# Performance work log

Hardware: AMD Instinct MI355X
Metric: run time of the kernel (lower is better)

The kernel has to match this reference:

```python
import jax, jax.numpy as jnp
import numpy as np

EPS = 1e-5
SLOPE = 0.01  # nn.LeakyReLU default
K = 32
SIGMA = 1.0

def lrelu(x):
    return jnp.where(x >= 0, x, SLOPE * x)

def bn(x, gamma, beta, axes):
    # BatchNorm in training mode (fresh module, batch statistics)
    mu = jnp.mean(x, axis=axes, keepdims=True)
    var = jnp.var(x, axis=axes, keepdims=True)
    return (x - mu) * jax.lax.rsqrt(var + EPS) * gamma + beta

def knn_gather(x, k):
    # x: (B, N, C) -> neighbor features (B, N, k, C) by smallest squared distance
    sq = jnp.sum(x * x, axis=-1)
    d = sq[:, :, None] - 2.0 * jnp.einsum('bnc,bmc->bnm', x, x) + sq[:, None, :]
    idx = jax.lax.top_k(-d, k)[1]                      # (B, N, k)
    nbr = jax.vmap(lambda xb, ib: xb[ib])(x, idx)      # (B, N, k, C)
    return nbr

def edge_conv(x, w1, g1, b1, w2, g2, b2):
    # DGCNN EdgeConv: feat = [x_j - x_i, x_i] -> 1x1 conv/BN/LeakyReLU x2 -> max over k
    nbr = knn_gather(x, K)                             # (B, N, k, C)
    xc = x[:, :, None, :]
    feat = jnp.concatenate([nbr - xc, jnp.broadcast_to(xc, nbr.shape)], axis=-1)
    h = lrelu(bn(jnp.einsum('bnkc,oc->bnko', feat, w1), g1, b1, (0, 1, 2)))
    h = lrelu(bn(jnp.einsum('bnkc,oc->bnko', h, w2), g2, b2, (0, 1, 2)))
    return jnp.max(h, axis=2)                          # (B, N, C_out)

def gaussian_kernel_conv(xnei, centers):
    # xnei: (B, N, k, C), centers: (O, C) -> (B, N, O)
    d = (jnp.sum(xnei * xnei, -1)[..., None]
         - 2.0 * jnp.einsum('bnkc,oc->bnko', xnei, centers)
         + jnp.sum(centers * centers, -1))
    return jnp.sum(jnp.exp(-d / (2.0 * SIGMA ** 2)), axis=2)

def setup_inputs() -> dict:
    key = jax.random.key(0)
    ks = jax.random.split(key, 16)
    s = 0.05
    return {
        'x': jax.random.normal(ks[0], (2, 3, 64, 64), jnp.float32),
        'kc_centers': jax.random.normal(ks[1], (128, 3), jnp.float32),
        'e1_w1': jax.random.normal(ks[2], (64, 6), jnp.float32) * s,
        'e1_g1': jnp.ones((64,), jnp.float32), 'e1_b1': jnp.zeros((64,), jnp.float32),
        'e1_w2': jax.random.normal(ks[3], (64, 64), jnp.float32) * s,
        'e1_g2': jnp.ones((64,), jnp.float32), 'e1_b2': jnp.zeros((64,), jnp.float32),
        'e2_w1': jax.random.normal(ks[4], (128, 128), jnp.float32) * s,
        'e2_g1': jnp.ones((128,), jnp.float32), 'e2_b1': jnp.zeros((128,), jnp.float32),
        'e2_w2': jax.random.normal(ks[5], (128, 128), jnp.float32) * s,
        'e2_g2': jnp.ones((128,), jnp.float32), 'e2_b2': jnp.zeros((128,), jnp.float32),
        'w1': jax.random.normal(ks[6], (1024, 256), jnp.float32) * s,
        'g1': jnp.ones((1024,), jnp.float32), 'b1': jnp.zeros((1024,), jnp.float32),
        'w2': jax.random.normal(ks[7], (512, 1024), jnp.float32) * s,
        'g2': jnp.ones((512,), jnp.float32), 'b2': jnp.zeros((512,), jnp.float32),
        'w3': jax.random.normal(ks[8], (256, 512), jnp.float32) * s,
        'g3': jnp.ones((256,), jnp.float32), 'b3': jnp.zeros((256,), jnp.float32),
        'w4': jax.random.normal(ks[9], (9, 256), jnp.float32) * s,
    }

def reference(x, kc_centers, e1_w1, e1_g1, e1_b1, e1_w2, e1_g2, e1_b2,
              e2_w1, e2_g1, e2_b1, e2_w2, e2_g2, e2_b2,
              w1, g1, b1, w2, g2, b2, w3, g3, b3, w4):
    bs, f, c, n = x.shape
    # knn over the (B, c*n, 3) point cloud
    pts = x.reshape(bs, -1, c * n).transpose(0, 2, 1)
    xnei = knn_gather(pts, K)                               # (B, c*n, K, 3)
    kernels = gaussian_kernel_conv(xnei, kc_centers)        # (B, c*n, 128)
    # EdgeConv chain on reshape-view (matches torch reshape semantics exactly)
    xe = x.reshape(bs, c * n, -1)                           # (B, c*n, 3)
    xe = edge_conv(xe, e1_w1, e1_g1, e1_b1, e1_w2, e1_g2, e1_b2)   # (B, c*n, 64)
    xe = edge_conv(xe, e2_w1, e2_g1, e2_b1, e2_w2, e2_g2, e2_b2)   # (B, c*n, 128)
    h = jnp.concatenate([xe.reshape(bs, -1, c, n),
                         kernels.transpose(0, 2, 1).reshape(bs, -1, c, n)], axis=1)  # (B,256,c,n)
    def cbr(h, w, g, b):
        h = jnp.einsum('bchw,oc->bohw', h, w)               # 1x1 conv, no bias
        return lrelu(bn(h, g[None, :, None, None], b[None, :, None, None], (0, 2, 3)))
    h = cbr(h, w1, g1, b1)
    h = cbr(h, w2, g2, b2)
    h = cbr(h, w3, g3, b3)
    h = jnp.einsum('bchw,oc->bohw', h, w4)                  # (B, 9, c, n)
    h = jnp.max(jnp.max(h, axis=3), axis=2)                 # (B, 9)
    out = h + jnp.eye(3, dtype=h.dtype).reshape(1, 9)
    return out.reshape(bs, 3, 3)
```

## Files before the change

kernel.cpp:

```cpp
#include <hip/hip_runtime.h>
#include <hip/hip_fp16.h>
#include <math.h>

#define WN 4096
#define NP 8192
#define KK 32
#define EPSB 1e-5f

typedef __attribute__((ext_vector_type(8))) short s8v;
typedef __attribute__((ext_vector_type(4))) float f4v;

__device__ __forceinline__ float lrelu(float x){ return fmaxf(x, 0.01f*x); }
__device__ __forceinline__ float rlane(float v, int c){
  return __int_as_float(__builtin_amdgcn_readlane(__float_as_int(v), c));
}
__device__ __forceinline__ short f2bf(float f){
  unsigned u = __float_as_uint(f);
  u = (u + 0x7fffu + ((u>>16)&1u)) >> 16;
  return (short)u;
}

__global__ void k_prep(const float* __restrict__ x, float* __restrict__ pts, float* __restrict__ xe0,
                       float* __restrict__ sqp, float* __restrict__ sqe,
                       float4* __restrict__ pts4, float4* __restrict__ xe04){
  int i = blockIdx.x*256 + threadIdx.x;
  if(i >= NP) return;
  int b = i>>12, p = i&4095;
  const float* xb = x + b*12288;
  float a0 = xb[p], a1 = xb[4096+p], a2 = xb[8192+p];
  pts[i*3+0]=a0; pts[i*3+1]=a1; pts[i*3+2]=a2;
  float sp = (a0*a0 + a1*a1) + a2*a2;
  sqp[i] = sp;
  pts4[i] = make_float4(a0,a1,a2,sp);
  float e0 = xb[p*3+0], e1 = xb[p*3+1], e2 = xb[p*3+2];
  xe0[i*3+0]=e0; xe0[i*3+1]=e1; xe0[i*3+2]=e2;
  float se = (e0*e0 + e1*e1) + e2*e2;
  sqe[i] = se;
  xe04[i] = make_float4(e0,e1,e2,se);
}

__device__ __forceinline__ void bitonic64(float& d, int& m, int l){
  #pragma unroll
  for(int k=2;k<=64;k<<=1){
    #pragma unroll
    for(int j=k>>1;j>0;j>>=1){
      float pd = __shfl_xor(d, j);
      int pm = __shfl_xor(m, j);
      bool pLess = (pd < d);
      bool dirUp = ((l & k) == 0);
      bool lower = ((l & j) == 0);
      bool take = dirUp ? (lower ? pLess : !pLess) : (lower ? !pLess : pLess);
      if(take){ d = pd; m = pm; }
    }
  }
}

__device__ __forceinline__ void topk_stream(float d, int m, int l, float& lv, int& li){
  unsigned long long mask = __ballot(d < rlane(lv, 31));
  while(mask){
    int s = __ffsll((unsigned long long)mask) - 1;
    float cd = __shfl(d, s);
    int cm = __shfl(m, s);
    unsigned long long less = __ballot(lv < cd);
    int pos = __popcll(less & 0xffffffffULL);
    float uv = __shfl_up(lv, 1);
    int ui = __shfl_up(li, 1);
    if(l < 32){
      if(l == pos){ lv = cd; li = cm; }
      else if(l > pos){ lv = uv; li = ui; }
    }
    mask &= mask - 1;
  }
}

__global__ __launch_bounds__(256) void k_knn3(const float4* __restrict__ pnt4, int* __restrict__ idx){
  int l = threadIdx.x&63;
  int q = blockIdx.x*4 + (threadIdx.x>>6);
  int b = q>>12, qr = q&4095;
  const float4* pb = pnt4 + ((size_t)b<<12);
  float4 qv = pb[qr];
  float q0=qv.x, q1=qv.y, q2=qv.z, sqq=qv.w;
  float4 nc = pb[l + 64];
  float dd; int mm = l;
  {
    float4 c = pb[l];
    float dot = q0*c.x + q1*c.y + q2*c.z;
    dd = (sqq - 2.0f*dot) + c.w;
  }
  bitonic64(dd, mm, l);
  float lv = (l<32) ? dd : 3.4e38f;
  int li = (l<32) ? mm : 0x7fffffff;
  #pragma unroll 4
  for(int j=1;j<64;j++){
    float4 c = nc;
    nc = pb[l + (((j+1)&63)<<6)];
    float dot = q0*c.x + q1*c.y + q2*c.z;
    float d = (sqq - 2.0f*dot) + c.w;
    topk_stream(d, l + (j<<6), l, lv, li);
  }
  if(l < 32) idx[(size_t)q*KK + l] = li;
}

__global__ __launch_bounds__(256) void k_knn_sel(const __half2* __restrict__ D, int* __restrict__ idx){
  int l = threadIdx.x&63;
  int q = blockIdx.x*4 + (threadIdx.x>>6);
  int b = q>>12, qr = q&4095;
  const __half2* row = D + ((size_t)b<<23) + ((size_t)qr<<11);
  __half2 h0 = row[l];
  __half2 nh = row[l + 64];
  float2 f0 = __half22float2(h0);
  float dmin, dmax; int mmin, mmax;
  if(f0.x <= f0.y){ dmin=f0.x; mmin=2*l;   dmax=f0.y; mmax=2*l+1; }
  else            { dmin=f0.y; mmin=2*l+1; dmax=f0.x; mmax=2*l;   }
  bitonic64(dmin, mmin, l);
  float lv = (l<32) ? dmin : 3.4e38f;
  int li = (l<32) ? mmin : 0x7fffffff;
  topk_stream(dmax, mmax, l, lv, li);
  #pragma unroll 4
  for(int j=1;j<32;j++){
    __half2 h = nh;
    nh = row[l + (((j+1)&31)<<6)];
    float2 g = __half22float2(h);
    int base = 2*(l + (j<<6));
    topk_stream(g.x, base,   l, lv, li);
    topk_stream(g.y, base+1, l, lv, li);
  }
  if(l < 32) idx[(size_t)q*KK + l] = li;
}

__global__ __launch_bounds__(128) void k_gauss(const float* __restrict__ pts, const float* __restrict__ sqp,
                                               const int* __restrict__ idxP, const float* __restrict__ cen,
                                               float* __restrict__ kout){
  __shared__ float nbx[KK], nby[KK], nbz[KK], nsq[KK];
  int p = blockIdx.x; int b = p>>12; int t = threadIdx.x;
  if(t < KK){
    int id = idxP[(size_t)p*KK + t] + (b<<12);
    nbx[t]=pts[id*3]; nby[t]=pts[id*3+1]; nbz[t]=pts[id*3+2];
    nsq[t]=sqp[id];
  }
  __syncthreads();
  float c0=cen[t*3], c1=cen[t*3+1], c2=cen[t*3+2];
  float sqc=(c0*c0+c1*c1)+c2*c2;
  float acc=0.f;
  #pragma unroll
  for(int k=0;k<KK;k++){
    float dot = nbx[k]*c0 + nby[k]*c1 + nbz[k]*c2;
    float d = (nsq[k] - 2.0f*dot) + sqc;
    acc += __expf(-0.5f*d);
  }
  kout[(size_t)((b<<7)+t)*4096 + (p&4095)] = acc;
}

__global__ void k_fin(const float* __restrict__ psum, const float* __restrict__ psq, int NW, int C, float Nn,
                      const float* __restrict__ g, const float* __restrict__ be,
                      float* __restrict__ sc, float* __restrict__ sh){
  int o = blockIdx.x, t = threadIdx.x;
  float s=0.f, q=0.f;
  for(int w=t; w<NW; w+=256){ s += psum[(size_t)w*C+o]; q += psq[(size_t)w*C+o]; }
  __shared__ float ls[256], lq[256];
  ls[t]=s; lq[t]=q; __syncthreads();
  for(int st=128; st; st>>=1){ if(t<st){ ls[t]+=ls[t+st]; lq[t]+=lq[t+st]; } __syncthreads(); }
  if(t==0){
    float mu = ls[0]/Nn;
    float var = lq[0]/Nn - mu*mu; if(var<0.f) var=0.f;
    float s1 = g[o]*rsqrtf(var + EPSB);
    sc[o]=s1; sh[o]=be[o]-mu*s1;
  }
}

__global__ __launch_bounds__(256) void k_ec1mom(const float* __restrict__ xe0, const int* __restrict__ idx1,
                                                float* __restrict__ pmom){
  int tid = blockIdx.x*256 + threadIdx.x;
  int l = threadIdx.x & 63;
  int wid = tid >> 6;
  float a[27];
  #pragma unroll
  for(int v=0;v<27;v++) a[v]=0.f;
  #pragma unroll
  for(int u=0;u<2;u++){
    int s = tid*2 + u;
    int p = s>>5;
    int bb = (p>>12)<<12;
    int id = bb + idx1[s];
    const float* nb = xe0 + (size_t)id*3;
    const float* xc = xe0 + (size_t)p*3;
    float f[6];
    f[0]=nb[0]-xc[0]; f[1]=nb[1]-xc[1]; f[2]=nb[2]-xc[2];
    f[3]=xc[0]; f[4]=xc[1]; f[5]=xc[2];
    int v=0;
    #pragma unroll
    for(int i=0;i<6;i++){
      #pragma unroll
      for(int j=i;j<6;j++){ a[v] = fmaf(f[i], f[j], a[v]); v++; }
    }
    #pragma unroll
    for(int i=0;i<6;i++) a[21+i] += f[i];
  }
  #pragma unroll
  for(int v=0;v<27;v++){
    float t = a[v];
    #pragma unroll
    for(int off=32; off; off>>=1) t += __shfl_xor(t, off);
    if(l==0) pmom[v*2048 + wid] = t;
  }
}

__global__ void k_msum(const float* __restrict__ pmom, float* __restrict__ mom){
  int v = blockIdx.x; int t = threadIdx.x;
  float s=0.f;
  for(int i=t;i<2048;i+=256) s += pmom[v*2048+i];
  __shared__ float ls[256];
  ls[t]=s; __syncthreads();
  for(int st=128; st; st>>=1){ if(t<st) ls[t]+=ls[t+st]; __syncthreads(); }
  if(t==0) mom[v]=ls[0];
}

__global__ void k_ec1bn(const float* __restrict__ mom, const float* __restrict__ w1,
                        const float* __restrict__ g, const float* __restrict__ be,
                        float* __restrict__ sc, float* __restrict__ sh){
  __shared__ float M[27];
  int t = threadIdx.x;
  if(t<27) M[t]=mom[t];
  __syncthreads();
  if(t<64){
    float w[6];
    #pragma unroll
    for(int c=0;c<6;c++) w[c]=w1[t*6+c];
    float qf=0.f, m1=0.f;
    int v=0;
    #pragma unroll
    for(int i=0;i<6;i++){
      #pragma unroll
      for(int j=i;j<6;j++){ qf += (i==j?1.f:2.f)*w[i]*w[j]*M[v]; v++; }
    }
    #pragma unroll
    for(int i=0;i<6;i++) m1 += w[i]*M[21+i];
    float N = 262144.f;
    float mu = m1/N;
    float var = qf/N - mu*mu; if(var<0.f) var=0.f;
    float s1 = g[t]*rsqrtf(var + EPSB);
    sc[t]=s1; sh[t]=be[t]-mu*s1;
  }
}

__global__ __launch_bounds__(256) void k_ec1g2(const float* __restrict__ xe0, const int* __restrict__ idx1,
                                               const float* __restrict__ w1, const float* __restrict__ w2T,
                                               const float* __restrict__ s1, const float* __restrict__ t1,
                                               float* __restrict__ h2m, float* __restrict__ psum,
                                               float* __restrict__ psq){
  __shared__ float As[64*64];
  __shared__ float Bs[64*132];
  __shared__ float feat[6][128];
  __shared__ float w1l[384];
  int t = threadIdx.x;
  int blk = blockIdx.x;
  int s0 = blk*128;
  int pbase = s0>>5;
  int bb = (s0>>17)<<12;
  #pragma unroll
  for(int i=0;i<16;i++) As[t + i*256] = w2T[t + i*256];
  for(int i=t; i<384; i+=256) w1l[i] = w1[i];
  if(t < 128){
    int s = s0 + t;
    int p = pbase + (t>>5);
    int id = bb + idx1[s];
    const float* nb = xe0 + (size_t)id*3;
    const float* xc = xe0 + (size_t)p*3;
    float x0 = xc[0], x1 = xc[1], x2 = xc[2];
    feat[0][t] = nb[0]-x0; feat[1][t] = nb[1]-x1; feat[2][t] = nb[2]-x2;
    feat[3][t] = x0; feat[4][t] = x1; feat[5][t] = x2;
  }
  __syncthreads();
  #pragma unroll
  for(int i=0;i<32;i++){
    int e = t + (i<<8);
    int k = e>>7, n = e&127;
    float h = w1l[k*6+0]*feat[0][n] + w1l[k*6+1]*feat[1][n] + w1l[k*6+2]*feat[2][n]
            + w1l[k*6+3]*feat[3][n] + w1l[k*6+4]*feat[4][n] + w1l[k*6+5]*feat[5][n];
    Bs[k*132 + n] = lrelu(fmaf(h, s1[k], t1[k]));
  }
  __syncthreads();
  int tx = t&15, ty = t>>4;
  float acc[4][8];
  #pragma unroll
  for(int i=0;i<4;i++){
    #pragma unroll
    for(int j=0;j<8;j++) acc[i][j]=0.f;
  }
  #pragma unroll 4
  for(int k=0;k<64;k++){
    float4 a  = *(const float4*)&As[k*64 + ty*4];
    float4 b0 = *(const float4*)&Bs[k*132 + tx*4];
    float4 b1 = *(const float4*)&Bs[k*132 + 64 + tx*4];
    float av[4] = {a.x,a.y,a.z,a.w};
    float bv[8] = {b0.x,b0.y,b0.z,b0.w,b1.x,b1.y,b1.z,b1.w};
    #pragma unroll
    for(int i=0;i<4;i++){
      #pragma unroll
      for(int j=0;j<8;j++) acc[i][j] = fmaf(av[i], bv[j], acc[i][j]);
    }
  }
  #pragma unroll
  for(int i=0;i<4;i++){
    int m = ty*4 + i;
    float sr = ((acc[i][0]+acc[i][1])+(acc[i][2]+acc[i][3])) + ((acc[i][4]+acc[i][5])+(acc[i][6]+acc[i][7]));
    float sq = ((acc[i][0]*acc[i][0]+acc[i][1]*acc[i][1])+(acc[i][2]*acc[i][2]+acc[i][3]*acc[i][3]))
             + ((acc[i][4]*acc[i][4]+acc[i][5]*acc[i][5])+(acc[i][6]*acc[i][6]+acc[i][7]*acc[i][7]));
    #pragma unroll
    for(int off=1; off<16; off<<=1){ sr += __shfl_xor(sr, off); sq += __shfl_xor(sq, off); }
    if(tx==0){ psum[(size_t)blk*64+m]=sr; psq[(size_t)blk*64+m]=sq; }
    float m0 = fmaxf(fmaxf(acc[i][0],acc[i][1]), fmaxf(acc[i][2],acc[i][3]));
    float m1 = fmaxf(fmaxf(acc[i][4],acc[i][5]), fmaxf(acc[i][6],acc[i][7]));
    #pragma unroll
    for(int off=1; off<8; off<<=1){ m0 = fmaxf(m0, __shfl_xor(m0, off)); m1 = fmaxf(m1, __shfl_xor(m1, off)); }
    if((tx&7)==0){
      int pl = pbase + (tx>>3);
      h2m[(size_t)pl*64 + m]     = m0;
      h2m[(size_t)(pl+2)*64 + m] = m1;
    }
  }
}

__global__ __launch_bounds__(256) void k_ec1fin(const float* __restrict__ h2m, const float* __restrict__ s2,
                                                const float* __restrict__ t2, float* __restrict__ xe1,
                                                float* __restrict__ xe1T, float* __restrict__ sqx){
  int gid = blockIdx.x*256 + threadIdx.x;
  int p = gid>>6, l = gid&63;
  float v = lrelu(fmaf(h2m[(size_t)p*64+l], s2[l], t2[l]));
  xe1[(size_t)p*64+l] = v;
  int b=p>>12, pr=p&4095;
  xe1T[(size_t)(b*64+l)*4096 + pr] = v;
  float sq = v*v;
  #pragma unroll
  for(int off=32; off; off>>=1) sq += __shfl_xor(sq, off);
  if(l==0) sqx[p]=sq;
}

__global__ __launch_bounds__(256) void k_dgemm_m(const short* __restrict__ X, const float* __restrict__ sqx,
                                                 __half* __restrict__ D){
  __shared__ short sA[8192], sB[8192];
  int t = threadIdx.x;
  int lane = t&63, w = t>>6;
  int wm4 = (w>>1)*4, wn4 = (w&1)*4;
  int mb = blockIdx.y, nb = blockIdx.x, b = blockIdx.z;
  const short* AG = X + (size_t)(b*32 + mb)*8192;
  const short* BG = X + (size_t)(b*32 + nb)*8192;
  #pragma unroll
  for(int i=0;i<4;i++){
    int slot = t + i*256;
    *(s8v*)&sA[slot*8] = *(const s8v*)&AG[slot*8];
    *(s8v*)&sB[slot*8] = *(const s8v*)&BG[slot*8];
  }
  __syncthreads();
  f4v acc[4][4];
  #pragma unroll
  for(int i=0;i<4;i++){
    #pragma unroll
    for(int j=0;j<4;j++) acc[i][j] = (f4v)(0.f);
  }
  #pragma unroll
  for(int kh=0;kh<2;kh++){
    s8v av[4], bv[4];
    #pragma unroll
    for(int f=0;f<4;f++) av[f] = *(const s8v*)&sA[(kh*8 + wm4 + f)*512 + lane*8];
    #pragma unroll
    for(int f=0;f<4;f++) bv[f] = *(const s8v*)&sB[(kh*8 + wn4 + f)*512 + lane*8];
    #pragma unroll
    for(int fm=0;fm<4;fm++){
      #pragma unroll
      for(int fn=0;fn<4;fn++)
        acc[fm][fn] = __builtin_amdgcn_mfma_f32_16x16x32_bf16(av[fm], bv[fn], acc[fm][fn], 0, 0, 0);
    }
  }
  const float* sb = sqx + (b<<12);
  __half* Db = D + ((size_t)b<<24);
  int l15 = lane&15, l4 = (lane>>4)*4;
  #pragma unroll
  for(int fm=0;fm<4;fm++){
    int m0 = mb*128 + wm4*16 + fm*16 + l4;
    float sm0 = sb[m0], sm1 = sb[m0+1], sm2 = sb[m0+2], sm3 = sb[m0+3];
    #pragma unroll
    for(int fn=0;fn<4;fn++){
      int n = nb*128 + wn4*16 + fn*16 + l15;
      float sqn = sb[n];
      __half2 h01 = __floats2half2_rn((sm0 + sqn) - 2.f*acc[fm][fn][0],
                                      (sm1 + sqn) - 2.f*acc[fm][fn][1]);
      __half2 h23 = __floats2half2_rn((sm2 + sqn) - 2.f*acc[fm][fn][2],
                                      (sm3 + sqn) - 2.f*acc[fm][fn][3]);
      __half2* p = (__half2*)&Db[(size_t)n*4096 + m0];
      p[0] = h01; p[1] = h23;
    }
  }
}

__global__ __launch_bounds__(256) void k_ec2m1(const float* __restrict__ xe1, const int* __restrict__ idx2,
                                               const short* __restrict__ wb, float* __restrict__ h1,
                                               float* __restrict__ psum, float* __restrict__ psq){
  __shared__ short sA[8192], sB[8192];
  __shared__ float cts[4][64];
  __shared__ int nid[128];
  __shared__ float srs[2][128], srq[2][128];
  int t = threadIdx.x;
  int blk = blockIdx.x;
  int s0 = blk*128;
  int pbase = s0>>5;
  int bb = (s0>>17)<<12;
  if(t<128) nid[t] = (idx2[s0+t] + bb)<<6;
  cts[t>>6][t&63] = xe1[(size_t)(pbase + (t>>6))*64 + (t&63)];
  int lane = t&63, w = t>>6;
  int wm4 = (w>>1)*4, wn4 = (w&1)*4;
  f4v acc[4][4];
  #pragma unroll
  for(int i=0;i<4;i++){
    #pragma unroll
    for(int j=0;j<4;j++) acc[i][j] = (f4v)(0.f);
  }
  for(int st=0; st<2; ++st){
    __syncthreads();
    #pragma unroll
    for(int i=0;i<4;i++){
      int slot = t + i*256;
      *(s8v*)&sA[slot*8] = *(const s8v*)&wb[st*8192 + slot*8];
      int chunk = slot>>6, li = slot&63;
      int n = (chunk&7)*16 + (li&15);
      int c = ((chunk>>3)<<5) + ((li>>4)<<3);
      float v[8];
      if(st==0){
        const float* src = xe1 + nid[n] + c;
        float4 a0 = *(const float4*)src;
        float4 a1 = *(const float4*)(src+4);
        const float* cc = &cts[n>>5][c];
        float4 c0 = *(const float4*)cc;
        float4 c1 = *(const float4*)(cc+4);
        v[0]=a0.x-c0.x; v[1]=a0.y-c0.y; v[2]=a0.z-c0.z; v[3]=a0.w-c0.w;
        v[4]=a1.x-c1.x; v[5]=a1.y-c1.y; v[6]=a1.z-c1.z; v[7]=a1.w-c1.w;
      } else {
        const float* cc = &cts[n>>5][c];
        float4 c0 = *(const float4*)cc;
        float4 c1 = *(const float4*)(cc+4);
        v[0]=c0.x; v[1]=c0.y; v[2]=c0.z; v[3]=c0.w;
        v[4]=c1.x; v[5]=c1.y; v[6]=c1.z; v[7]=c1.w;
      }
      s8v r;
      #pragma unroll
      for(int j=0;j<8;j++) r[j] = f2bf(v[j]);
      *(s8v*)&sB[slot*8] = r;
    }
    __syncthreads();
    #pragma unroll
    for(int kh=0;kh<2;kh++){
      s8v av[4], bv[4];
      #pragma unroll
      for(int f=0;f<4;f++) av[f] = *(const s8v*)&sA[(kh*8 + wm4 + f)*512 + lane*8];
      #pragma unroll
      for(int f=0;f<4;f++) bv[f] = *(const s8v*)&sB[(kh*8 + wn4 + f)*512 + lane*8];
      #pragma unroll
      for(int fm=0;fm<4;fm++){
        #pragma unroll
        for(int fn=0;fn<4;fn++)
          acc[fm][fn] = __builtin_amdgcn_mfma_f32_16x16x32_bf16(av[fm], bv[fn], acc[fm][fn], 0, 0, 0);
      }
    }
  }
  int l15 = lane&15, l4 = (lane>>4)<<2;
  #pragma unroll
  for(int fm=0;fm<4;fm++){
    int mb_ = wm4*16 + fm*16 + l4;
    #pragma unroll
    for(int fn=0;fn<4;fn++){
      int n = wn4*16 + fn*16 + l15;
      *(float4*)&h1[(size_t)(s0+n)*128 + mb_] =
        make_float4(acc[fm][fn][0], acc[fm][fn][1], acc[fm][fn][2], acc[fm][fn][3]);
    }
    #pragma unroll
    for(int r=0;r<4;r++){
      float sr = (acc[fm][0][r]+acc[fm][1][r]) + (acc[fm][2][r]+acc[fm][3][r]);
      float sq = (acc[fm][0][r]*acc[fm][0][r]+acc[fm][1][r]*acc[fm][1][r])
               + (acc[fm][2][r]*acc[fm][2][r]+acc[fm][3][r]*acc[fm][3][r]);
      #pragma unroll
      for(int off=1; off<16; off<<=1){ sr += __shfl_xor(sr, off); sq += __shfl_xor(sq, off); }
      if(l15==0){ srs[w&1][mb_+r] = sr; srq[w&1][mb_+r] = sq; }
    }
  }
  __syncthreads();
  if(t<128){
    psum[(size_t)blk*128+t] = srs[0][t]+srs[1][t];
    psq[(size_t)blk*128+t]  = srq[0][t]+srq[1][t];
  }
}

__global__ __launch_bounds__(256) void k_ec2m2(const float* __restrict__ h1, const short* __restrict__ wb,
                                               const float* __restrict__ s1, const float* __restrict__ t1,
                                               float* __restrict__ h2max, float* __restrict__ psum,
                                               float* __restrict__ psq){
  __shared__ short sA[8192], sB[8192];
  __shared__ float bnS[128], bnT[128];
  __shared__ float srs[2][128], srq[2][128];
  int t = threadIdx.x;
  int blk = blockIdx.x;
  int s0 = blk*128;
  int pbase = s0>>5;
  if(t<128){ bnS[t]=s1[t]; bnT[t]=t1[t]; }
  int lane = t&63, w = t>>6;
  int wm4 = (w>>1)*4, wn4 = (w&1)*4;
  f4v acc[4][4];
  #pragma unroll
  for(int i=0;i<4;i++){
    #pragma unroll
    for(int j=0;j<4;j++) acc[i][j] = (f4v)(0.f);
  }
  for(int st=0; st<2; ++st){
    __syncthreads();
    #pragma unroll
    for(int i=0;i<4;i++){
      int slot = t + i*256;
      *(s8v*)&sA[slot*8] = *(const s8v*)&wb[st*8192 + slot*8];
      int chunk = slot>>6, li = slot&63;
      int n = (chunk&7)*16 + (li&15);
      int c = st*64 + ((chunk>>3)<<5) + ((li>>4)<<3);
      const float* src = h1 + (size_t)(s0+n)*128 + c;
      float4 a0 = *(const float4*)src;
      float4 a1 = *(const float4*)(src+4);
      float v[8] = {a0.x,a0.y,a0.z,a0.w,a1.x,a1.y,a1.z,a1.w};
      s8v r;
      #pragma unroll
      for(int j=0;j<8;j++) r[j] = f2bf(lrelu(fmaf(v[j], bnS[c+j], bnT[c+j])));
      *(s8v*)&sB[slot*8] = r;
    }
    __syncthreads();
    #pragma unroll
    for(int kh=0;kh<2;kh++){
      s8v av[4], bv[4];
      #pragma unroll
      for(int f=0;f<4;f++) av[f] = *(const s8v*)&sA[(kh*8 + wm4 + f)*512 + lane*8];
      #pragma unroll
      for(int f=0;f<4;f++) bv[f] = *(const s8v*)&sB[(kh*8 + wn4 + f)*512 + lane*8];
      #pragma unroll
      for(int fm=0;fm<4;fm++){
        #pragma unroll
        for(int fn=0;fn<4;fn++)
          acc[fm][fn] = __builtin_amdgcn_mfma_f32_16x16x32_bf16(av[fm], bv[fn], acc[fm][fn], 0, 0, 0);
      }
    }
  }
  int l15 = lane&15, l4 = (lane>>4)<<2;
  int pp0 = wn4>>1;
  #pragma unroll
  for(int fm=0;fm<4;fm++){
    int mb_ = wm4*16 + fm*16 + l4;
    #pragma unroll
    for(int r=0;r<4;r++){
      float sr = (acc[fm][0][r]+acc[fm][1][r]) + (acc[fm][2][r]+acc[fm][3][r]);
      float sq = (acc[fm][0][r]*acc[fm][0][r]+acc[fm][1][r]*acc[fm][1][r])
               + (acc[fm][2][r]*acc[fm][2][r]+acc[fm][3][r]*acc[fm][3][r]);
      float m0 = fmaxf(acc[fm][0][r], acc[fm][1][r]);
      float m1 = fmaxf(acc[fm][2][r], acc[fm][3][r]);
      #pragma unroll
      for(int off=1; off<16; off<<=1){ sr += __shfl_xor(sr, off); sq += __shfl_xor(sq, off); }
      #pragma unroll
      for(int off=1; off<16; off<<=1){ m0 = fmaxf(m0, __shfl_xor(m0, off)); m1 = fmaxf(m1, __shfl_xor(m1, off)); }
      if(l15==0){
        srs[w&1][mb_+r] = sr; srq[w&1][mb_+r] = sq;
        h2max[(size_t)(pbase+pp0)*128   + mb_+r] = m0;
        h2max[(size_t)(pbase+pp0+1)*128 + mb_+r] = m1;
      }
    }
  }
  __syncthreads();
  if(t<128){
    psum[(size_t)blk*128+t] = srs[0][t]+srs[1][t];
    psq[(size_t)blk*128+t]  = srq[0][t]+srq[1][t];
  }
}

__global__ void k_xe2fin(float* __restrict__ xe2, const float* __restrict__ s2, const float* __restrict__ t2){
  int i = blockIdx.x*256 + threadIdx.x;
  if(i >= NP*128) return;
  int o = i&127;
  xe2[i] = lrelu(fmaf(xe2[i], s2[o], t2[o]));
}

__global__ void k_transpose(const float* __restrict__ w, float* __restrict__ wT, int O, int C){
  int i = blockIdx.x*256 + threadIdx.x;
  if(i >= O*C) return;
  int o = i / C, c = i % C;
  wT[(size_t)c*O + o] = w[i];
}

__global__ void k_wprep(const float* __restrict__ w, short* __restrict__ wb, int M, int K){
  int tid = blockIdx.x*256 + threadIdx.x;
  int m = tid % M, kb8 = tid / M;
  int k0 = kb8*8;
  float4 v0 = *(const float4*)&w[(size_t)m*K + k0];
  float4 v1 = *(const float4*)&w[(size_t)m*K + k0 + 4];
  s8v r;
  r[0]=f2bf(v0.x); r[1]=f2bf(v0.y); r[2]=f2bf(v0.z); r[3]=f2bf(v0.w);
  r[4]=f2bf(v1.x); r[5]=f2bf(v1.y); r[6]=f2bf(v1.z); r[7]=f2bf(v1.w);
  int region = (m>>7)*(K>>6) + (k0>>6);
  int chunk = ((kb8>>2)&1)*8 + ((m>>4)&7);
  int lane = (kb8&3)*16 + (m&15);
  *(s8v*)&wb[(size_t)region*8192 + chunk*512 + lane*8] = r;
}

__global__ void k_bprep(const float* __restrict__ in, const float* __restrict__ sc, const float* __restrict__ sh,
                        short* __restrict__ ob, int K){
  int tid = blockIdx.x*256 + threadIdx.x;
  int n = tid & 8191, kb8 = tid >> 13;
  int k0 = kb8*8;
  int b = n>>12, s = n&4095;
  const float* ib = in + ((size_t)b*K + k0)*4096 + s;
  float v[8];
  #pragma unroll
  for(int j=0;j<8;j++) v[j] = ib[(size_t)j*4096];
  if(sc){
    #pragma unroll
    for(int j=0;j<8;j++) v[j] = lrelu(fmaf(v[j], sc[k0+j], sh[k0+j]));
  }
  s8v r;
  #pragma unroll
  for(int j=0;j<8;j++) r[j] = f2bf(v[j]);
  int region = (n>>7)*(K>>6) + (k0>>6);
  int chunk = ((kb8>>2)&1)*8 + ((n>>4)&7);
  int lane = (kb8&3)*16 + (n&15);
  *(s8v*)&ob[(size_t)region*8192 + chunk*512 + lane*8] = r;
}

__global__ void k_bprep1(const float* __restrict__ xe2, const float* __restrict__ kr,
                         short* __restrict__ ob){
  int tid = blockIdx.x*256 + threadIdx.x;
  int n = tid & 8191, kb8 = tid >> 13;
  int k0 = kb8*8;
  int b = n>>12, s = n&4095;
  const float* ib;
  if(k0 < 128) ib = xe2 + (size_t)b*524288 + (size_t)k0*4096 + s;
  else         ib = kr + ((size_t)(b*128 + (k0-128)))*4096 + s;
  float v[8];
  #pragma unroll
  for(int j=0;j<8;j++) v[j] = ib[(size_t)j*4096];
  s8v r;
  #pragma unroll
  for(int j=0;j<8;j++) r[j] = f2bf(v[j]);
  int region = (n>>7)*4 + (k0>>6);
  int chunk = ((kb8>>2)&1)*8 + ((n>>4)&7);
  int lane = (kb8&3)*16 + (n&15);
  *(s8v*)&ob[(size_t)region*8192 + chunk*512 + lane*8] = r;
}

__global__ __launch_bounds__(256) void k_gmm(const short* __restrict__ A, const short* __restrict__ B,
                                             float* __restrict__ out, int M, int K){
  __shared__ short sA[8192], sB[8192];
  int t = threadIdx.x;
  int lane = t&63;
  int w = t>>6;
  int wm4 = (w>>1)*4, wn4 = (w&1)*4;
  int mb = blockIdx.y, nb = blockIdx.x;
  int ksteps = K>>6;
  const short* AG = A + (size_t)mb*ksteps*8192;
  const short* BG = B + (size_t)nb*ksteps*8192;
  f4v acc[4][4];
  #pragma unroll
  for(int i=0;i<4;i++){
    #pragma unroll
    for(int j=0;j<4;j++) acc[i][j] = (f4v)(0.f);
  }
  for(int st=0; st<ksteps; ++st){
    __syncthreads();
    #pragma unroll
    for(int i=0;i<4;i++){
      int slot = t + i*256;
      *(s8v*)&sA[slot*8] = *(const s8v*)&AG[(size_t)st*8192 + slot*8];
      *(s8v*)&sB[slot*8] = *(const s8v*)&BG[(size_t)st*8192 + slot*8];
    }
    __syncthreads();
    #pragma unroll
    for(int kh=0;kh<2;kh++){
      s8v av[4], bv[4];
      #pragma unroll
      for(int f=0;f<4;f++) av[f] = *(const s8v*)&sA[(kh*8 + wm4 + f)*512 + lane*8];
      #pragma unroll
      for(int f=0;f<4;f++) bv[f] = *(const s8v*)&sB[(kh*8 + wn4 + f)*512 + lane*8];
      #pragma unroll
      for(int fm=0;fm<4;fm++){
        #pragma unroll
        for(int fn=0;fn<4;fn++)
          acc[fm][fn] = __builtin_amdgcn_mfma_f32_16x16x32_bf16(av[fm], bv[fn], acc[fm][fn], 0, 0, 0);
      }
    }
  }
  int l15 = lane&15, l4 = (lane>>4)*4;
  #pragma unroll
  for(int fm=0;fm<4;fm++){
    int mrow = mb*128 + wm4*16 + fm*16 + l4;
    #pragma unroll
    for(int fn=0;fn<4;fn++){
      int n = nb*128 + wn4*16 + fn*16 + l15;
      int b = n>>12, s = n&4095;
      float* ob = out + ((size_t)b*M + mrow)*4096 + s;
      #pragma unroll
      for(int r=0;r<4;r++) ob[(size_t)r*4096] = acc[fm][fn][r];
    }
  }
}

__global__ void k_cstats(const float* __restrict__ buf, int C, const float* __restrict__ g,
                         const float* __restrict__ be, float* __restrict__ sc, float* __restrict__ sh){
  int o = blockIdx.x, t = threadIdx.x;
  float s=0.f, q=0.f;
  for(int i=t;i<8192;i+=256){
    int b=i>>12, ss_=i&4095;
    float v = buf[(size_t)(b*C+o)*4096 + ss_];
    s+=v; q+=v*v;
  }
  __shared__ float ls[256], lq[256];
  ls[t]=s; lq[t]=q; __syncthreads();
  for(int st=128; st; st>>=1){ if(t<st){ ls[t]+=ls[t+st]; lq[t]+=lq[t+st]; } __syncthreads(); }
  if(t==0){
    float mu = ls[0]/8192.f;
    float var = lq[0]/8192.f - mu*mu; if(var<0.f) var=0.f;
    float s1 = g[o]*rsqrtf(var + EPSB);
    sc[o]=s1; sh[o]=be[o]-mu*s1;
  }
}

__global__ __launch_bounds__(256) void k_final4(const float* __restrict__ c3, const float* __restrict__ w4T,
                                                const float* __restrict__ sc, const float* __restrict__ sh,
                                                float* __restrict__ pmax){
  int b = blockIdx.y, st = blockIdx.x;
  int t = threadIdx.x; int s = st*256 + t;
  float acc[9];
  #pragma unroll
  for(int j=0;j<9;j++) acc[j]=0.f;
  const float* ib = c3 + (size_t)b*256*4096;
  for(int c=0;c<256;c++){
    float x = lrelu(fmaf(ib[(size_t)c*4096+s], sc[c], sh[c]));
    #pragma unroll
    for(int j=0;j<9;j++) acc[j]=fmaf(x, w4T[c*9+j], acc[j]);
  }
  __shared__ float red[256];
  for(int j=0;j<9;j++){
    red[t]=acc[j]; __syncthreads();
    for(int stp=128; stp; stp>>=1){ if(t<stp) red[t]=fmaxf(red[t],red[t+stp]); __syncthreads(); }
    if(t==0) pmax[(b*16+st)*9 + j]=red[0];
    __syncthreads();
  }
}

__global__ void k_out(const float* __restrict__ pmax, float* __restrict__ out){
  int i = threadIdx.x;
  if(i<18){
    int b=i/9, o=i%9;
    float m=-3.4e38f;
    for(int k=0;k<16;k++) m=fmaxf(m, pmax[(b*16+k)*9+o]);
    out[i] = m + ((o==0||o==4||o==8)?1.f:0.f);
  }
}

extern "C" void kernel_launch(void* const* d_in, const int* in_sizes, int n_in,
                              void* d_out, int out_size, void* d_ws, size_t ws_size,
                              hipStream_t stream){
  const float* x    = (const float*)d_in[0];
  const float* kc   = (const float*)d_in[1];
  const float* e1w1 = (const float*)d_in[2];
  const float* e1g1 = (const float*)d_in[3];
  const float* e1b1 = (const float*)d_in[4];
  const float* e1w2 = (const float*)d_in[5];
  const float* e1g2 = (const float*)d_in[6];
  const float* e1b2 = (const float*)d_in[7];
  const float* e2w1 = (const float*)d_in[8];
  const float* e2g1 = (const float*)d_in[9];
  const float* e2b1 = (const float*)d_in[10];
  const float* e2w2 = (const float*)d_in[11];
  const float* e2g2 = (const float*)d_in[12];
  const float* e2b2 = (const float*)d_in[13];
  const float* w1   = (const float*)d_in[14];
  const float* g1   = (const float*)d_in[15];
  const float* b1   = (const float*)d_in[16];
  const float* w2   = (const float*)d_in[17];
  const float* g2   = (const float*)d_in[18];
  const float* b2   = (const float*)d_in[19];
  const float* w3   = (const float*)d_in[20];
  const float* g3   = (const float*)d_in[21];
  const float* b3   = (const float*)d_in[22];
  const float* w4   = (const float*)d_in[23];

  if(ws_size < 156061696ull) return;
  char* ws = (char*)d_ws;
  float* pts   = (float*)(ws + 0);
  float* xe0   = (float*)(ws + 98304);
  float* sqp   = (float*)(ws + 196608);
  float* sqe   = (float*)(ws + 229376);
  float* sqx1  = (float*)(ws + 262144);
  float* xe1   = (float*)(ws + 294912);
  float* xe1T  = (float*)(ws + 2392064);
  float* xe2   = (float*)(ws + 4489216);
  float* kr    = (float*)(ws + 8683520);
  int*   idxP  = (int*)  (ws + 12877824);
  int*   idx1  = (int*)  (ws + 13926400);
  int*   idx2  = (int*)  (ws + 14974976);
  float* psum  = (float*)(ws + 16023552);
  float* psq   = (float*)(ws + 17072128);
  float* par   = (float*)(ws + 18120704);
  float* pmax  = (float*)(ws + 18153472);
  float* e1w2T = (float*)(ws + 18157568);
  float* wT4   = (float*)(ws + 21827584);
  float* hbuf  = (float*)(ws + 21843968);
  short* wbe1  = (short*)(ws + 0);
  short* wbe2  = (short*)(ws + 65536);
  float4* pts4 = (float4*)(ws + 4489216);
  float4* xe04 = (float4*)(ws + 4489216 + 131072);
  short* actB  = (short*)(ws + 88952832);
  short* xpack = (short*)(ws + 88952832);
  short* wb1   = (short*)(ws + 105730048);
  short* wb2   = (short*)(ws + 106254336);
  short* wb3   = (short*)(ws + 107302912);
  float* pmom  = psum;
  float* momv  = psq;

  float* e1s1 = par+0;    float* e1t1 = par+64;
  float* e1s2 = par+128;  float* e1t2 = par+192;
  float* e2s1 = par+256;  float* e2t1 = par+384;
  float* e2s2 = par+512;  float* e2t2 = par+640;
  float* c1s  = par+768;  float* c1t  = par+1792;
  float* c2s  = par+2816; float* c2t  = par+3328;
  float* c3s  = par+3840; float* c3t  = par+4096;

  float* c1out = hbuf + 2097152;
  float* c2out = hbuf + 10485760;
  float* c3out = hbuf + 14680064;

  hipLaunchKernelGGL(k_prep, dim3(32), dim3(256), 0, stream, x, pts, xe0, sqp, sqe, pts4, xe04);
  hipLaunchKernelGGL(k_knn3, dim3(2048), dim3(256), 0, stream, pts4, idxP);
  hipLaunchKernelGGL(k_knn3, dim3(2048), dim3(256), 0, stream, xe04, idx1);
  hipLaunchKernelGGL(k_gauss, dim3(8192), dim3(128), 0, stream, pts, sqp, idxP, kc, kr);

  hipLaunchKernelGGL(k_transpose, dim3(16), dim3(256), 0, stream, e1w2, e1w2T, 64, 64);
  hipLaunchKernelGGL(k_ec1mom, dim3(512), dim3(256), 0, stream, xe0, idx1, pmom);
  hipLaunchKernelGGL(k_msum, dim3(27), dim3(256), 0, stream, pmom, momv);
  hipLaunchKernelGGL(k_ec1bn, dim3(1), dim3(64), 0, stream, momv, e1w1, e1g1, e1b1, e1s1, e1t1);
  hipLaunchKernelGGL(k_ec1g2, dim3(2048), dim3(256), 0, stream, xe0, idx1, e1w1, e1w2T, e1s1, e1t1, hbuf, psum, psq);
  hipLaunchKernelGGL(k_fin, dim3(64), dim3(256), 0, stream, psum, psq, 2048, 64, 262144.f, e1g2, e1b2, e1s2, e1t2);
  hipLaunchKernelGGL(k_ec1fin, dim3(2048), dim3(256), 0, stream, hbuf, e1s2, e1t2, xe1, xe1T, sqx1);

  hipLaunchKernelGGL(k_wprep, dim3(256), dim3(256), 0, stream, xe1, xpack, 8192, 64);
  hipLaunchKernelGGL(k_dgemm_m, dim3(32,32,2), dim3(256), 0, stream, xpack, sqx1, (__half*)hbuf);
  hipLaunchKernelGGL(k_knn_sel, dim3(2048), dim3(256), 0, stream, (const __half2*)hbuf, idx2);

  hipLaunchKernelGGL(k_wprep, dim3(8), dim3(256), 0, stream, e2w1, wbe1, 128, 128);
  hipLaunchKernelGGL(k_wprep, dim3(8), dim3(256), 0, stream, e2w2, wbe2, 128, 128);
  hipLaunchKernelGGL(k_ec2m1, dim3(2048), dim3(256), 0, stream, xe1, idx2, wbe1, hbuf, psum, psq);
  hipLaunchKernelGGL(k_fin, dim3(128), dim3(256), 0, stream, psum, psq, 2048, 128, 262144.f, e2g1, e2b1, e2s1, e2t1);
  hipLaunchKernelGGL(k_ec2m2, dim3(2048), dim3(256), 0, stream, hbuf, wbe2, e2s1, e2t1, xe2, psum, psq);
  hipLaunchKernelGGL(k_fin, dim3(128), dim3(256), 0, stream, psum, psq, 2048, 128, 262144.f, e2g2, e2b2, e2s2, e2t2);
  hipLaunchKernelGGL(k_xe2fin, dim3(4096), dim3(256), 0, stream, xe2, e2s2, e2t2);

  hipLaunchKernelGGL(k_wprep, dim3(128), dim3(256), 0, stream, w1, wb1, 1024, 256);
  hipLaunchKernelGGL(k_wprep, dim3(256), dim3(256), 0, stream, w2, wb2, 512, 1024);
  hipLaunchKernelGGL(k_wprep, dim3(64),  dim3(256), 0, stream, w3, wb3, 256, 512);
  hipLaunchKernelGGL(k_transpose, dim3((9*256+255)/256), dim3(256), 0, stream, w4, wT4, 9, 256);

  hipLaunchKernelGGL(k_bprep1, dim3(1024), dim3(256), 0, stream, xe2, kr, actB);
  hipLaunchKernelGGL(k_gmm, dim3(64,8), dim3(256), 0, stream, wb1, actB, c1out, 1024, 256);
  hipLaunchKernelGGL(k_cstats, dim3(1024), dim3(256), 0, stream, c1out, 1024, g1, b1, c1s, c1t);

  hipLaunchKernelGGL(k_bprep, dim3(4096), dim3(256), 0, stream, c1out, c1s, c1t, actB, 1024);
  hipLaunchKernelGGL(k_gmm, dim3(64,4), dim3(256), 0, stream, wb2, actB, c2out, 512, 1024);
  hipLaunchKernelGGL(k_cstats, dim3(512), dim3(256), 0, stream, c2out, 512, g2, b2, c2s, c2t);

  hipLaunchKernelGGL(k_bprep, dim3(2048), dim3(256), 0, stream, c2out, c2s, c2t, actB, 512);
  hipLaunchKernelGGL(k_gmm, dim3(64,2), dim3(256), 0, stream, wb3, actB, c3out, 256, 512);
  hipLaunchKernelGGL(k_cstats, dim3(256), dim3(256), 0, stream, c3out, 256, g3, b3, c3s, c3t);

  hipLaunchKernelGGL(k_final4, dim3(16,2), dim3(256), 0, stream, c3out, wT4, c3s, c3t, pmax);
  hipLaunchKernelGGL(k_out, dim3(1), dim3(32), 0, stream, pmax, (float*)d_out);
}
```

Before: 626.3 us.

## Process two kNN queries per wavefront using half-wave top-k lists

The kNN selection kernels now assign two queries to each 64-lane wavefront, one per 32-lane half. Each half keeps its own sorted top-32 list, and the initial sort shrinks from a 64-wide to a 32-wide bitonic sort. The streaming insertion handles one candidate from each half per iteration, so the upper 32 lanes no longer sit idle holding the list. The aim is to halve the wavefront count and stop wasting half of every wave. In exchange, each insertion iteration costs more shuffles, and the loop runs as long as whichever half has more inserts.

```diff
diff --git a/kernel.cpp b/kernel.cpp
--- a/kernel.cpp
+++ b/kernel.cpp
@@ -39,93 +39,102 @@
   xe04[i] = make_float4(e0,e1,e2,se);
 }
 
-__device__ __forceinline__ void bitonic64(float& d, int& m, int l){
-  #pragma unroll
-  for(int k=2;k<=64;k<<=1){
+__device__ __forceinline__ void bitonic32(float& d, int& m, int lp){
+  #pragma unroll
+  for(int k=2;k<=32;k<<=1){
     #pragma unroll
     for(int j=k>>1;j>0;j>>=1){
       float pd = __shfl_xor(d, j);
       int pm = __shfl_xor(m, j);
       bool pLess = (pd < d);
-      bool dirUp = ((l & k) == 0);
-      bool lower = ((l & j) == 0);
+      bool dirUp = ((lp & k) == 0);
+      bool lower = ((lp & j) == 0);
       bool take = dirUp ? (lower ? pLess : !pLess) : (lower ? !pLess : pLess);
       if(take){ d = pd; m = pm; }
     }
   }
 }
 
-__device__ __forceinline__ void topk_stream(float d, int m, int l, float& lv, int& li){
-  unsigned long long mask = __ballot(d < rlane(lv, 31));
+__device__ __forceinline__ void topk2(float d, int m, int l, float& lv, int& li){
+  bool low = (l < 32);
+  float thrA = rlane(lv, 31), thrB = rlane(lv, 63);
+  unsigned long long mask = __ballot(d < (low ? thrA : thrB));
   while(mask){
-    int s = __ffsll((unsigned long long)mask) - 1;
-    float cd = __shfl(d, s);
-    int cm = __shfl(m, s);
+    unsigned mA = (unsigned)mask, mB = (unsigned)(mask>>32);
+    int sa = mA ? (__ffs(mA)-1)  : 0;
+    int sb = mB ? (__ffs(mB)+31) : 0;
+    float ca = __shfl(d, sa); int ia = __shfl(m, sa);
+    float cb = __shfl(d, sb); int ib = __shfl(m, sb);
+    float cdA = mA ? ca : 3.4e38f;
+    float cdB = mB ? cb : 3.4e38f;
+    float cd = low ? cdA : cdB;
+    int cm = low ? ia : ib;
     unsigned long long less = __ballot(lv < cd);
-    int pos = __popcll(less & 0xffffffffULL);
-    float uv = __shfl_up(lv, 1);
-    int ui = __shfl_up(li, 1);
-    if(l < 32){
-      if(l == pos){ lv = cd; li = cm; }
-      else if(l > pos){ lv = uv; li = ui; }
-    }
-    mask &= mask - 1;
+    int pos = low ? __popc((unsigned)less) : __popc((unsigned)(less>>32));
+    float uv = __shfl_up(lv, 1, 32);
+    int ui = __shfl_up(li, 1, 32);
+    int p = l&31;
+    if(p == pos){ lv = cd; li = cm; }
+    else if(p > pos){ lv = uv; li = ui; }
+    mA &= mA-1; mB &= mB-1;
+    mask = (unsigned long long)mA | (((unsigned long long)mB)<<32);
   }
 }
 
 __global__ __launch_bounds__(256) void k_knn3(const float4* __restrict__ pnt4, int* __restrict__ idx){
   int l = threadIdx.x&63;
-  int q = blockIdx.x*4 + (threadIdx.x>>6);
+  int lp = l&31;
+  int q = blockIdx.x*8 + (threadIdx.x>>6)*2 + ((l>>5)&1);
   int b = q>>12, qr = q&4095;
   const float4* pb = pnt4 + ((size_t)b<<12);
   float4 qv = pb[qr];
   float q0=qv.x, q1=qv.y, q2=qv.z, sqq=qv.w;
-  float4 nc = pb[l + 64];
-  float dd; int mm = l;
+  float4 nc = pb[lp + 32];
+  float lv; int li;
   {
-    float4 c = pb[l];
+    float4 c = pb[lp];
     float dot = q0*c.x + q1*c.y + q2*c.z;
-    dd = (sqq - 2.0f*dot) + c.w;
-  }
-  bitonic64(dd, mm, l);
-  float lv = (l<32) ? dd : 3.4e38f;
-  int li = (l<32) ? mm : 0x7fffffff;
+    float dd = (sqq - 2.0f*dot) + c.w;
+    int mm = lp;
+    bitonic32(dd, mm, lp);
+    lv = dd; li = mm;
+  }
+  #pragma unroll 4
+  for(int j=1;j<128;j++){
+    float4 c = nc;
+    nc = pb[lp + (((j+1)&127)<<5)];
+    float dot = q0*c.x + q1*c.y + q2*c.z;
+    float d = (sqq - 2.0f*dot) + c.w;
+    topk2(d, lp + (j<<5), l, lv, li);
+  }
+  idx[(size_t)q*KK + lp] = li;
+}
+
+__global__ __launch_bounds__(256) void k_knn_sel(const __half2* __restrict__ D, int* __restrict__ idx){
+  int l = threadIdx.x&63;
+  int lp = l&31;
+  int q = blockIdx.x*8 + (threadIdx.x>>6)*2 + ((l>>5)&1);
+  int b = q>>12, qr = q&4095;
+  const __half2* row = D + ((size_t)b<<23) + ((size_t)qr<<11);
+  __half2 h0 = row[lp];
+  __half2 nh = row[lp + 32];
+  float2 f0 = __half22float2(h0);
+  float dmin, dmax; int mmin, mmax;
+  if(f0.x <= f0.y){ dmin=f0.x; mmin=2*lp;   dmax=f0.y; mmax=2*lp+1; }
+  else            { dmin=f0.y; mmin=2*lp+1; dmax=f0.x; mmax=2*lp;   }
+  bitonic32(dmin, mmin, lp);
+  float lv = dmin; int li = mmin;
+  topk2(dmax, mmax, l, lv, li);
   #pragma unroll 4
   for(int j=1;j<64;j++){
-    float4 c = nc;
-    nc = pb[l + (((j+1)&63)<<6)];
-    float dot = q0*c.x + q1*c.y + q2*c.z;
-    float d = (sqq - 2.0f*dot) + c.w;
-    topk_stream(d, l + (j<<6), l, lv, li);
-  }
-  if(l < 32) idx[(size_t)q*KK + l] = li;
-}
-
-__global__ __launch_bounds__(256) void k_knn_sel(const __half2* __restrict__ D, int* __restrict__ idx){
-  int l = threadIdx.x&63;
-  int q = blockIdx.x*4 + (threadIdx.x>>6);
-  int b = q>>12, qr = q&4095;
-  const __half2* row = D + ((size_t)b<<23) + ((size_t)qr<<11);
-  __half2 h0 = row[l];
-  __half2 nh = row[l + 64];
-  float2 f0 = __half22float2(h0);
-  float dmin, dmax; int mmin, mmax;
-  if(f0.x <= f0.y){ dmin=f0.x; mmin=2*l;   dmax=f0.y; mmax=2*l+1; }
-  else            { dmin=f0.y; mmin=2*l+1; dmax=f0.x; mmax=2*l;   }
-  bitonic64(dmin, mmin, l);
-  float lv = (l<32) ? dmin : 3.4e38f;
-  int li = (l<32) ? mmin : 0x7fffffff;
-  topk_stream(dmax, mmax, l, lv, li);
-  #pragma unroll 4
-  for(int j=1;j<32;j++){
     __half2 h = nh;
-    nh = row[l + (((j+1)&31)<<6)];
+    nh = row[lp + (((j+1)&63)<<5)];
     float2 g = __half22float2(h);
-    int base = 2*(l + (j<<6));
-    topk_stream(g.x, base,   l, lv, li);
-    topk_stream(g.y, base+1, l, lv, li);
-  }
-  if(l < 32) idx[(size_t)q*KK + l] = li;
+    int base = 2*(lp + (j<<5));
+    topk2(g.x, base,   l, lv, li);
+    topk2(g.y, base+1, l, lv, li);
+  }
+  idx[(size_t)q*KK + lp] = li;
 }
 
 __global__ __launch_bounds__(128) void k_gauss(const float* __restrict__ pts, const float* __restrict__ sqp,
@@ -829,8 +838,8 @@
   float* c3out = hbuf + 14680064;
 
   hipLaunchKernelGGL(k_prep, dim3(32), dim3(256), 0, stream, x, pts, xe0, sqp, sqe, pts4, xe04);
-  hipLaunchKernelGGL(k_knn3, dim3(2048), dim3(256), 0, stream, pts4, idxP);
-  hipLaunchKernelGGL(k_knn3, dim3(2048), dim3(256), 0, stream, xe04, idx1);
+  hipLaunchKernelGGL(k_knn3, dim3(1024), dim3(256), 0, stream, pts4, idxP);
+  hipLaunchKernelGGL(k_knn3, dim3(1024), dim3(256), 0, stream, xe04, idx1);
   hipLaunchKernelGGL(k_gauss, dim3(8192), dim3(128), 0, stream, pts, sqp, idxP, kc, kr);
 
   hipLaunchKernelGGL(k_transpose, dim3(16), dim3(256), 0, stream, e1w2, e1w2T, 64, 64);
@@ -843,7 +852,7 @@
 
   hipLaunchKernelGGL(k_wprep, dim3(256), dim3(256), 0, stream, xe1, xpack, 8192, 64);
   hipLaunchKernelGGL(k_dgemm_m, dim3(32,32,2), dim3(256), 0, stream, xpack, sqx1, (__half*)hbuf);
-  hipLaunchKernelGGL(k_knn_sel, dim3(2048), dim3(256), 0, stream, (const __half2*)hbuf, idx2);
+  hipLaunchKernelGGL(k_knn_sel, dim3(1024), dim3(256), 0, stream, (const __half2*)hbuf, idx2);
 
   hipLaunchKernelGGL(k_wprep, dim3(8), dim3(256), 0, stream, e2w1, wbe1, 128, 128);
   hipLaunchKernelGGL(k_wprep, dim3(8), dim3(256), 0, stream, e2w2, wbe2, 128, 128);
```

Result: slower. 663.5 us (+5.9%).

## Buffer top-k candidates in shared memory and merge with bitonic sort

Applied to the files above, without the earlier changes.

Replaces the per-candidate serial insertion into the wave's top-32 list with a per-wave shared-memory buffer. Surviving candidates are compacted into it by ballot and prefix count. When the buffer reaches 32 entries it is merged with the current list by a 64-wide bitonic sort, which also tightens the threshold. This cuts the number of serialized shuffle/ballot insertion steps per candidate. The cost is a full bitonic merge per 32 survivors, and the threshold goes stale between merges, so more candidates get buffered.

```diff
diff --git a/kernel.cpp b/kernel.cpp
--- a/kernel.cpp
+++ b/kernel.cpp
@@ -55,29 +55,50 @@
   }
 }
 
-__device__ __forceinline__ void topk_stream(float d, int m, int l, float& lv, int& li){
-  unsigned long long mask = __ballot(d < rlane(lv, 31));
+__device__ __forceinline__ void kmerge(const float2* __restrict__ buf, int cnt, int l,
+                                       float& lv, int& li){
+  __builtin_amdgcn_wave_barrier();
+  float md; int mi;
+  if(l < 32){ md = lv; mi = li; }
+  else{
+    int i = l - 32;
+    if(i < cnt){ float2 e = buf[i]; md = e.x; mi = __float_as_int(e.y); }
+    else{ md = 3.4e38f; mi = 0x7fffffff; }
+  }
+  bitonic64(md, mi, l);
+  if(l < 32){ lv = md; li = mi; }
+}
+
+__device__ __forceinline__ void topk_buf(float d, int m, int l, float2* __restrict__ buf,
+                                         int& cnt, float& thr, float& lv, int& li){
+  bool alive = d < thr;
+  unsigned long long mask = __ballot(alive);
   while(mask){
-    int s = __ffsll((unsigned long long)mask) - 1;
-    float cd = __shfl(d, s);
-    int cm = __shfl(m, s);
-    unsigned long long less = __ballot(lv < cd);
-    int pos = __popcll(less & 0xffffffffULL);
-    float uv = __shfl_up(lv, 1);
-    int ui = __shfl_up(li, 1);
-    if(l < 32){
-      if(l == pos){ lv = cd; li = cm; }
-      else if(l > pos){ lv = uv; li = ui; }
-    }
-    mask &= mask - 1;
+    int nsurv = __popcll(mask);
+    int space = 32 - cnt;
+    int prefix = __popcll(mask & ((1ull<<l)-1ull));
+    bool store = alive && (prefix < space);
+    if(store) buf[cnt + prefix] = make_float2(d, __int_as_float(m));
+    cnt += (nsurv < space) ? nsurv : space;
+    alive = alive && !store;
+    if(cnt == 32){
+      kmerge(buf, 32, l, lv, li);
+      cnt = 0;
+      thr = rlane(lv, 31);
+      alive = alive && (d < thr);
+    }
+    mask = __ballot(alive);
   }
 }
 
 __global__ __launch_bounds__(256) void k_knn3(const float4* __restrict__ pnt4, int* __restrict__ idx){
+  __shared__ float2 bufs[4][32];
   int l = threadIdx.x&63;
-  int q = blockIdx.x*4 + (threadIdx.x>>6);
+  int wid = threadIdx.x>>6;
+  int q = blockIdx.x*4 + wid;
   int b = q>>12, qr = q&4095;
   const float4* pb = pnt4 + ((size_t)b<<12);
+  float2* buf = bufs[wid];
   float4 qv = pb[qr];
   float q0=qv.x, q1=qv.y, q2=qv.z, sqq=qv.w;
   float4 nc = pb[l + 64];
@@ -90,22 +111,28 @@
   bitonic64(dd, mm, l);
   float lv = (l<32) ? dd : 3.4e38f;
   int li = (l<32) ? mm : 0x7fffffff;
+  float thr = rlane(lv, 31);
+  int cnt = 0;
   #pragma unroll 4
   for(int j=1;j<64;j++){
     float4 c = nc;
     nc = pb[l + (((j+1)&63)<<6)];
     float dot = q0*c.x + q1*c.y + q2*c.z;
     float d = (sqq - 2.0f*dot) + c.w;
-    topk_stream(d, l + (j<<6), l, lv, li);
-  }
+    topk_buf(d, l + (j<<6), l, buf, cnt, thr, lv, li);
+  }
+  if(cnt) kmerge(buf, cnt, l, lv, li);
   if(l < 32) idx[(size_t)q*KK + l] = li;
 }
 
 __global__ __launch_bounds__(256) void k_knn_sel(const __half2* __restrict__ D, int* __restrict__ idx){
+  __shared__ float2 bufs[4][32];
   int l = threadIdx.x&63;
-  int q = blockIdx.x*4 + (threadIdx.x>>6);
+  int wid = threadIdx.x>>6;
+  int q = blockIdx.x*4 + wid;
   int b = q>>12, qr = q&4095;
   const __half2* row = D + ((size_t)b<<23) + ((size_t)qr<<11);
+  float2* buf = bufs[wid];
   __half2 h0 = row[l];
   __half2 nh = row[l + 64];
   float2 f0 = __half22float2(h0);
@@ -115,16 +142,19 @@
   bitonic64(dmin, mmin, l);
   float lv = (l<32) ? dmin : 3.4e38f;
   int li = (l<32) ? mmin : 0x7fffffff;
-  topk_stream(dmax, mmax, l, lv, li);
+  float thr = rlane(lv, 31);
+  int cnt = 0;
+  topk_buf(dmax, mmax, l, buf, cnt, thr, lv, li);
   #pragma unroll 4
   for(int j=1;j<32;j++){
     __half2 h = nh;
     nh = row[l + (((j+1)&31)<<6)];
     float2 g = __half22float2(h);
     int base = 2*(l + (j<<6));
-    topk_stream(g.x, base,   l, lv, li);
-    topk_stream(g.y, base+1, l, lv, li);
-  }
+    topk_buf(g.x, base,   l, buf, cnt, thr, lv, li);
+    topk_buf(g.y, base+1, l, buf, cnt, thr, lv, li);
+  }
+  if(cnt) kmerge(buf, cnt, l, lv, li);
   if(l < 32) idx[(size_t)q*KK + l] = li;
 }
 
```

Result: faster. 543.4 us (-13.2%).
